# Kernel tuning notes

Hardware: AMD Instinct MI355X
Metric: run time of the kernel (lower is better)

The kernel has to match this reference:

```python
import jax, jax.numpy as jnp
import numpy as np

EPS = 1e-5

def conv(x, w, groups=1):
    # x: NCHW, w: OIHW, VALID padding, stride 1 (cross-correlation, same as torch conv2d)
    return jax.lax.conv_general_dilated(x, w, (1, 1), 'VALID',
                                        feature_group_count=groups,
                                        dimension_numbers=('NCHW', 'OIHW', 'NCHW'))

def bn(x, g, b, m, v):
    # eval-mode batchnorm with running stats
    scale = (g / jnp.sqrt(v + EPS))[None, :, None, None]
    return (x - m[None, :, None, None]) * scale + b[None, :, None, None]

def xcorr_depthwise(x, k):
    # x: [B,C,Hs,Ws] search, k: [B,C,Hk,Wk] per-sample kernels
    B, C, H, W = x.shape
    xr = x.reshape(1, B * C, H, W)
    kr = k.reshape(B * C, 1, k.shape[2], k.shape[3])
    out = conv(xr, kr, groups=B * C)  # [1, B*C, Ho, Wo]
    return out.reshape(B, C, out.shape[2], out.shape[3])

def setup_inputs() -> dict:
    key = jax.random.key(0)
    ks = jax.random.split(key, 16)
    Cin, Hid, Cout = 256, 256, 20
    inp = {
        'kernel': jax.random.normal(ks[0], (128, Cin, 7, 7), jnp.float32),
        'search': jax.random.normal(ks[1], (128, Cin, 31, 31), jnp.float32),
        'wk': jax.random.normal(ks[2], (Hid, Cin, 3, 3), jnp.float32) * 0.02,
        'gk': jnp.ones((Hid,), jnp.float32),
        'bk': jnp.zeros((Hid,), jnp.float32),
        'mk': jax.random.normal(ks[3], (Hid,), jnp.float32) * 0.1,
        'vk': jax.random.uniform(ks[4], (Hid,), jnp.float32) + 0.5,
        'ws': jax.random.normal(ks[5], (Hid, Cin, 3, 3), jnp.float32) * 0.02,
        'gs': jnp.ones((Hid,), jnp.float32),
        'bs': jnp.zeros((Hid,), jnp.float32),
        'ms': jax.random.normal(ks[6], (Hid,), jnp.float32) * 0.1,
        'vs': jax.random.uniform(ks[7], (Hid,), jnp.float32) + 0.5,
        'wh1': jax.random.normal(ks[8], (Hid, Hid, 1, 1), jnp.float32) * 0.02,
        'gh': jnp.ones((Hid,), jnp.float32),
        'bh': jnp.zeros((Hid,), jnp.float32),
        'mh': jax.random.normal(ks[9], (Hid,), jnp.float32) * 0.1,
        'vh': jax.random.uniform(ks[10], (Hid,), jnp.float32) + 0.5,
        'wh2': jax.random.normal(ks[11], (Cout, Hid, 1, 1), jnp.float32) * 0.02,
        'bh2': jnp.zeros((Cout,), jnp.float32),
    }
    return inp

def reference(kernel, search, wk, gk, bk, mk, vk, ws, gs, bs, ms, vs,
              wh1, gh, bh, mh, vh, wh2, bh2):
    k = jax.nn.relu(bn(conv(kernel, wk), gk, bk, mk, vk))   # [B,256,5,5]
    s = jax.nn.relu(bn(conv(search, ws), gs, bs, ms, vs))   # [B,256,29,29]
    f = xcorr_depthwise(s, k)                               # [B,256,25,25]
    h = jax.nn.relu(bn(conv(f, wh1), gh, bh, mh, vh))
    out = conv(h, wh2) + bh2[None, :, None, None]           # [B,20,25,25]
    return out
```

## Files before the change

### kernel.cpp

```cpp
#include <hip/hip_runtime.h>

typedef __bf16 bf16x8 __attribute__((ext_vector_type(8)));
typedef float floatx4 __attribute__((ext_vector_type(4)));
typedef unsigned short u16;
typedef unsigned int u32;

__device__ __forceinline__ u16 f2bf(float f) {
    union { float f; unsigned int u; } q; q.f = f;
    unsigned int r = q.u + 0x7FFFu + ((q.u >> 16) & 1u);
    return (u16)(r >> 16);
}
__device__ __forceinline__ float bf2f(u16 b) {
    union { unsigned int u; float f; } q; q.u = ((unsigned int)b) << 16;
    return q.f;
}

__device__ __forceinline__ void gl2lds16(const u16* g, u16* l) {
    __builtin_amdgcn_global_load_lds((const __attribute__((address_space(1))) u32*)g,
                                     (__attribute__((address_space(3))) u32*)l, 16, 0, 0);
}


__global__ __launch_bounds__(256) void bn_prep(
    const float* __restrict__ gk, const float* __restrict__ bk,
    const float* __restrict__ mk, const float* __restrict__ vk,
    const float* __restrict__ gs, const float* __restrict__ bs,
    const float* __restrict__ ms, const float* __restrict__ vs,
    const float* __restrict__ gh, const float* __restrict__ bh,
    const float* __restrict__ mh, const float* __restrict__ vh,
    float* __restrict__ par)
{
    int i = threadIdx.x;
    float s;
    s = gk[i] * rsqrtf(vk[i] + 1e-5f); par[0*256+i] = s; par[1*256+i] = bk[i] - mk[i]*s;
    s = gs[i] * rsqrtf(vs[i] + 1e-5f); par[2*256+i] = s; par[3*256+i] = bs[i] - ms[i]*s;
    s = gh[i] * rsqrtf(vh[i] + 1e-5f); par[4*256+i] = s; par[5*256+i] = bh[i] - mh[i]*s;
}

__global__ __launch_bounds__(256) void pack3x3(const float* __restrict__ w, u16* __restrict__ out) {
    int tid = blockIdx.x * 256 + threadIdx.x;
    int o  = tid / 2304;
    int k  = tid - o * 2304;
    int rc = k >> 8;
    int ci = k & 255;
    out[tid] = f2bf(w[o * 2304 + ci * 9 + rc]);
}

__global__ __launch_bounds__(256) void cast_bf16(const float* __restrict__ in, u16* __restrict__ out, int n) {
    int tid = blockIdx.x * 256 + threadIdx.x;
    if (tid < n) out[tid] = f2bf(in[tid]);
}

__global__ __launch_bounds__(256) void nchw2nhwc_t(const float* __restrict__ in, u16* __restrict__ out,
                                                   int HW, int sptiles) {
    __shared__ float tile[64][33];
    int bid = blockIdx.x;
    int st  = bid % sptiles;
    int tmp = bid / sptiles;
    int ct  = tmp & 3;
    int b   = tmp >> 2;
    int sp0 = st * 32, ci0 = ct * 64;
    int t = threadIdx.x;
    int j = t & 31, i8 = t >> 5;
    const float* ip = in + ((size_t)b * 256 + ci0 + i8) * HW + sp0 + j;
#pragma unroll
    for (int k = 0; k < 8; ++k) {
        if (sp0 + j < HW) tile[i8 + k * 8][j] = ip[(size_t)(k * 8) * HW];
    }
    __syncthreads();
    int cl = t & 63, s4 = t >> 6;
#pragma unroll
    for (int k = 0; k < 8; ++k) {
        int spl = s4 + k * 4;
        int sp  = sp0 + spl;
        if (sp < HW) out[((size_t)b * HW + sp) * 256 + ci0 + cl] = f2bf(tile[cl][spl]);
    }
}

__global__ __launch_bounds__(256) void conv_gemm(
    const u16* __restrict__ Ain, const u16* __restrict__ Wpk,
    const float* __restrict__ scale, const float* __restrict__ shift,
    u16* __restrict__ Out,
    int OHW, int OW, int IW, int bstride, int KW, int nrc, int mblocks)
{
    __shared__ u16 Alds[4096];
    __shared__ u16 Blds[4096];

    const int tot = mblocks * 2;
    const int grp = (tot >> 3) << 3;
    const int lid = blockIdx.x;
    const int nid = (lid < grp) ? ((lid & 7) * (grp >> 3) + (lid >> 3)) : lid;
    const int m0 = (nid >> 1) * 128;
    const int n0 = (nid & 1) * 128;

    const int t    = threadIdx.x;
    const int wave = t >> 6;
    const int lane = t & 63;
    const int quad = lane >> 4;
    const int lrow = lane & 15;

    const int koff = (((t & 3) ^ ((t >> 3) & 3)) << 3);
    const int r0 = t >> 2;
    int m_a0 = m0 + r0;
    int b0 = m_a0 / OHW; int rem0 = m_a0 - b0 * OHW; int y0 = rem0 / OW; int x0 = rem0 - y0 * OW;
    int m_a1 = m_a0 + 64;
    int b1 = m_a1 / OHW; int rem1 = m_a1 - b1 * OHW; int y1 = rem1 / OW; int x1 = rem1 - y1 * OW;
    const u16* ag0 = Ain + (size_t)b0 * bstride + (size_t)(y0 * IW + x0) * 256 + koff;
    const u16* ag1 = Ain + (size_t)b1 * bstride + (size_t)(y1 * IW + x1) * 256 + koff;
    const int Ktot = nrc * 256;
    const u16* bg0 = Wpk + (size_t)(n0 + r0) * Ktot + koff;
    const u16* bg1 = bg0 + (size_t)64 * Ktot;

    u16* lA0 = Alds + wave * 512;
    u16* lA1 = Alds + 2048 + wave * 512;
    u16* lB0 = Blds + wave * 512;
    u16* lB1 = Blds + 2048 + wave * 512;

    floatx4 zero = {0.f, 0.f, 0.f, 0.f};
    floatx4 acc[4][4];
#pragma unroll
    for (int i = 0; i < 4; ++i)
#pragma unroll
        for (int j = 0; j < 4; ++j) acc[i][j] = zero;

    const int wr  = (wave >> 1) << 6;
    const int wc  = (wave & 1) << 6;
    const int pos = ((quad ^ ((lrow >> 1) & 3)) << 3);

    const int nchunks = nrc << 3;
    for (int ch = 0; ch < nchunks; ++ch) {
        int rc  = ch >> 3;
        int ci0 = (ch & 7) << 5;
        int rr  = rc / KW;
        int cc  = rc - rr * KW;
        int ao  = (rr * IW + cc) * 256 + ci0;
        int bo  = ch << 5;
        __syncthreads();
        gl2lds16(ag0 + ao, lA0);
        gl2lds16(ag1 + ao, lA1);
        gl2lds16(bg0 + bo, lB0);
        gl2lds16(bg1 + bo, lB1);
        __syncthreads();
        bf16x8 af[4], bfr[4];
#pragma unroll
        for (int mi = 0; mi < 4; ++mi)
            af[mi] = *(const bf16x8*)&Alds[(wr + mi * 16 + lrow) * 32 + pos];
#pragma unroll
        for (int ni = 0; ni < 4; ++ni)
            bfr[ni] = *(const bf16x8*)&Blds[(wc + ni * 16 + lrow) * 32 + pos];
#pragma unroll
        for (int mi = 0; mi < 4; ++mi)
#pragma unroll
            for (int ni = 0; ni < 4; ++ni)
                acc[mi][ni] = __builtin_amdgcn_mfma_f32_16x16x32_bf16(af[mi], bfr[ni], acc[mi][ni], 0, 0, 0);
    }

    float sc[4], sh[4];
#pragma unroll
    for (int ni = 0; ni < 4; ++ni) {
        int gn = n0 + wc + ni * 16 + lrow;
        sc[ni] = scale[gn];
        sh[ni] = shift[gn];
    }
#pragma unroll
    for (int mi = 0; mi < 4; ++mi) {
        int gm = m0 + wr + mi * 16 + (quad << 2);
#pragma unroll
        for (int ri = 0; ri < 4; ++ri) {
            size_t ro = (size_t)(gm + ri) * 256 + n0 + wc + lrow;
#pragma unroll
            for (int ni = 0; ni < 4; ++ni) {
                float v = acc[mi][ni][ri] * sc[ni] + sh[ni];
                v = fmaxf(v, 0.f);
                Out[ro + ni * 16] = f2bf(v);
            }
        }
    }
}

__global__ __launch_bounds__(512, 2) void conv_gemm256(
    const u16* __restrict__ Ain, const u16* __restrict__ Wpk,
    const float* __restrict__ scale, const float* __restrict__ shift,
    u16* __restrict__ Out,
    int OHW, int OW, int IW, int bstride, int KW, int NKT, int Mtot)
{
    __shared__ __align__(16) u16 Alds[2][256][64];
    __shared__ __align__(16) u16 Blds[2][256][64];

    const int Ktot = NKT << 6;

    const int nblk = gridDim.x;
    const int lid = blockIdx.x;
    const int q8 = nblk >> 3, r8 = nblk & 7;
    const int xcd = lid & 7, sub = lid >> 3;
    const int nid = (xcd < r8) ? (xcd * (q8 + 1) + sub)
                               : (r8 * (q8 + 1) + (xcd - r8) * q8 + sub);
    const int m0 = nid << 8;

    const int t     = threadIdx.x;
    const int wave  = t >> 6;
    const int lane  = t & 63;
    const int lrow  = lane & 15;
    const int lquad = lane >> 4;
    const int wmBase = (wave >> 2) << 7;
    const int wnBase = (wave & 3) << 6;

    const u16* pA[4];
    const u16* pB[4];
#pragma unroll
    for (int j = 0; j < 4; ++j) {
        int u = j * 512 + t;
        int row = u >> 3, slot = u & 7;
        int ko = ((slot ^ (row & 7)) << 3);
        int m = m0 + row; if (m >= Mtot) m = Mtot - 1;
        int b = m / OHW; int rem = m - b * OHW; int y = rem / OW; int x = rem - y * OW;
        pA[j] = Ain + (size_t)b * bstride + (size_t)(y * IW + x) * 256 + ko;
        pB[j] = Wpk + (size_t)row * (size_t)Ktot + ko;
    }

    const int xo0 = ((lquad ^ (lrow & 7)) << 3);
    const int xo1 = xo0 ^ 32;

    floatx4 acc[8][4];
#pragma unroll
    for (int i = 0; i < 8; ++i)
#pragma unroll
        for (int j = 0; j < 4; ++j) acc[i][j] = (floatx4){0.f, 0.f, 0.f, 0.f};

#pragma unroll
    for (int j = 0; j < 4; ++j)
        gl2lds16(pA[j], &Alds[0][0][0] + j * 4096 + wave * 512);
#pragma unroll
    for (int j = 0; j < 4; ++j)
        gl2lds16(pB[j], &Blds[0][0][0] + j * 4096 + wave * 512);
    asm volatile("s_waitcnt vmcnt(0)" ::: "memory");
    __builtin_amdgcn_s_barrier();

#define LOADA(mb) do {                                              \
        const u16* _p = Ab + (wmBase + (mb) * 16 + lrow) * 64;      \
        aF[0][0] = *(const bf16x8*)(_p + xo0);                      \
        aF[0][1] = *(const bf16x8*)(_p + xo1);                      \
        aF[1][0] = *(const bf16x8*)(_p + 1024 + xo0);               \
        aF[1][1] = *(const bf16x8*)(_p + 1024 + xo1);               \
    } while (0)

#define MFMA16(mb) do {                                                                               \
        _Pragma("unroll")                                                                             \
        for (int _n = 0; _n < 4; ++_n) {                                                              \
            acc[(mb)][_n]     = __builtin_amdgcn_mfma_f32_16x16x32_bf16(aF[0][0], bB[_n][0], acc[(mb)][_n], 0, 0, 0);     \
            acc[(mb)][_n]     = __builtin_amdgcn_mfma_f32_16x16x32_bf16(aF[0][1], bB[_n][1], acc[(mb)][_n], 0, 0, 0);     \
            acc[(mb) + 1][_n] = __builtin_amdgcn_mfma_f32_16x16x32_bf16(aF[1][0], bB[_n][0], acc[(mb) + 1][_n], 0, 0, 0); \
            acc[(mb) + 1][_n] = __builtin_amdgcn_mfma_f32_16x16x32_bf16(aF[1][1], bB[_n][1], acc[(mb) + 1][_n], 0, 0, 0); \
        }                                                                                             \
    } while (0)

#define PH_MID() do {                                        \
        __builtin_amdgcn_s_barrier();                        \
        asm volatile("s_waitcnt lgkmcnt(0)" ::: "memory");   \
        __builtin_amdgcn_s_setprio(1);                       \
    } while (0)

#define PH_END() do {                                        \
        __builtin_amdgcn_s_setprio(0);                       \
        __builtin_amdgcn_s_barrier();                        \
    } while (0)

#pragma unroll 2
    for (int kt = 0; kt < NKT; ++kt) {
        const int c = kt & 1;
        const u16* Ab = &Alds[c][0][0];
        const u16* Bb = &Blds[c][0][0];
        u16* An = &Alds[c ^ 1][0][0];
        u16* Bn = &Blds[c ^ 1][0][0];
        const int pf = (kt + 1 < NKT);
        const int kt1 = kt + 1;
        const int rc = kt1 >> 2;
        const int rr = rc / KW;
        const int cc = rc - rr * KW;
        const int aoffA = (rr * IW + cc) * 256 + ((kt1 & 3) << 6);
        const int boffB = kt1 << 6;

        bf16x8 bB[4][2];
        bf16x8 aF[2][2];

#pragma unroll
        for (int ni = 0; ni < 4; ++ni) {
            const u16* _p = Bb + (wnBase + ni * 16 + lrow) * 64;
            bB[ni][0] = *(const bf16x8*)(_p + xo0);
            bB[ni][1] = *(const bf16x8*)(_p + xo1);
        }
        LOADA(0);
        if (pf) {
#pragma unroll
            for (int j = 0; j < 4; ++j)
                gl2lds16(pA[j] + aoffA, An + j * 4096 + wave * 512);
        }
        PH_MID();
        MFMA16(0);
        PH_END();

        LOADA(2);
        if (pf) {
#pragma unroll
            for (int j = 0; j < 4; ++j)
                gl2lds16(pB[j] + boffB, Bn + j * 4096 + wave * 512);
        }
        PH_MID();
        MFMA16(2);
        PH_END();

        LOADA(4);
        PH_MID();
        MFMA16(4);
        PH_END();

        LOADA(6);
        PH_MID();
        MFMA16(6);
        __builtin_amdgcn_s_setprio(0);
        asm volatile("s_waitcnt vmcnt(0)" ::: "memory");
        __builtin_amdgcn_s_barrier();
    }

#undef LOADA
#undef MFMA16
#undef PH_MID
#undef PH_END

    float sc[4], sh[4];
#pragma unroll
    for (int ni = 0; ni < 4; ++ni) {
        int gn = wnBase + ni * 16 + lrow;
        sc[ni] = scale[gn];
        sh[ni] = shift[gn];
    }
#pragma unroll
    for (int mi = 0; mi < 8; ++mi) {
        int gm0 = m0 + wmBase + mi * 16 + (lquad << 2);
#pragma unroll
        for (int ri = 0; ri < 4; ++ri) {
            int gm = gm0 + ri;
            if (gm < Mtot) {
                size_t ro = (size_t)gm * 256 + wnBase + lrow;
#pragma unroll
                for (int ni = 0; ni < 4; ++ni) {
                    float v = acc[mi][ni][ri] * sc[ni] + sh[ni];
                    v = fmaxf(v, 0.f);
                    Out[ro + ni * 16] = f2bf(v);
                }
            }
        }
    }
}

__global__ __launch_bounds__(256) void xcorr(const u16* __restrict__ ss, const u16* __restrict__ kk,
                                             u16* __restrict__ f) {
    int bid = blockIdx.x;
    int b = bid / 25, y = bid - b * 25;
    int ci = threadIdx.x;
    float kv[25];
#pragma unroll
    for (int i = 0; i < 25; ++i)
        kv[i] = bf2f(kk[(size_t)(b * 25 + i) * 256 + ci]);
    const u16* sbase = ss + (size_t)(b * 29 + y) * 29 * 256 + ci;
    u16* fbase = f + (size_t)(b * 25 + y) * 25 * 256 + ci;
    for (int x = 0; x < 25; ++x) {
        float acc = 0.f;
#pragma unroll
        for (int r = 0; r < 5; ++r)
#pragma unroll
            for (int c = 0; c < 5; ++c)
                acc += bf2f(sbase[(r * 29 + x + c) * 256]) * kv[r * 5 + c];
        fbase[x * 256] = f2bf(acc);
    }
}

__global__ __launch_bounds__(256) void head(const u16* __restrict__ h, const float* __restrict__ w2,
                                            const float* __restrict__ b2, float* __restrict__ out) {
    __shared__ u16   hl[25 * 264];
    __shared__ float wl[20 * 257];
    int bid = blockIdx.x;
    int b = bid / 25, y = bid - b * 25;
    int t = threadIdx.x;
    const u16* hrow = h + (size_t)(b * 25 + y) * 25 * 256;
    for (int i = t; i < 6400; i += 256) {
        int x = i >> 8, c = i & 255;
        hl[x * 264 + c] = hrow[i];
    }
    for (int i = t; i < 5120; i += 256) {
        int co = i >> 8, c = i & 255;
        wl[co * 257 + c] = w2[i];
    }
    __syncthreads();
    for (int o = t; o < 500; o += 256) {
        int x = o / 20, co = o - x * 20;
        float acc = b2[co];
        const u16* hp = &hl[x * 264];
        const float* wp = &wl[co * 257];
        for (int k = 0; k < 256; ++k) acc += bf2f(hp[k]) * wp[k];
        out[(size_t)((b * 20 + co) * 25 + y) * 25 + x] = acc;
    }
}

#define OFF_SIN  0ull
#define SZ_SIN   62980096ull
#define OFF_KIN  (OFF_SIN + SZ_SIN)
#define SZ_KIN   3211264ull
#define OFF_WKP  (OFF_KIN + SZ_KIN)
#define SZ_WKP   1179648ull
#define OFF_WSP  (OFF_WKP + SZ_WKP)
#define SZ_WSP   1179648ull
#define OFF_WH1P (OFF_WSP + SZ_WSP)
#define SZ_WH1P  131072ull
#define OFF_PAR  (OFF_WH1P + SZ_WH1P)
#define SZ_PAR   8192ull
#define OFF_KK   (OFF_PAR + SZ_PAR)
#define SZ_KK    1638400ull
#define OFF_SS   (OFF_KK + SZ_KK)
#define SZ_SS    55115776ull
#define OFF_F    OFF_SIN
#define OFF_H    OFF_SS

extern "C" void kernel_launch(void* const* d_in, const int* in_sizes, int n_in,
                              void* d_out, int out_size, void* d_ws, size_t ws_size,
                              hipStream_t stream) {
    const float* kin  = (const float*)d_in[0];
    const float* sin_ = (const float*)d_in[1];
    const float* wk   = (const float*)d_in[2];
    const float* gk   = (const float*)d_in[3];
    const float* bk   = (const float*)d_in[4];
    const float* mk   = (const float*)d_in[5];
    const float* vk   = (const float*)d_in[6];
    const float* wsw  = (const float*)d_in[7];
    const float* gs   = (const float*)d_in[8];
    const float* bs   = (const float*)d_in[9];
    const float* ms   = (const float*)d_in[10];
    const float* vs   = (const float*)d_in[11];
    const float* wh1  = (const float*)d_in[12];
    const float* gh   = (const float*)d_in[13];
    const float* bh   = (const float*)d_in[14];
    const float* mh   = (const float*)d_in[15];
    const float* vh   = (const float*)d_in[16];
    const float* wh2  = (const float*)d_in[17];
    const float* bh2  = (const float*)d_in[18];
    float* out = (float*)d_out;

    char* w = (char*)d_ws;
    u16*   SIN  = (u16*)(w + OFF_SIN);
    u16*   KIN  = (u16*)(w + OFF_KIN);
    u16*   WKP  = (u16*)(w + OFF_WKP);
    u16*   WSP  = (u16*)(w + OFF_WSP);
    u16*   WH1P = (u16*)(w + OFF_WH1P);
    float* PAR  = (float*)(w + OFF_PAR);
    u16*   KK   = (u16*)(w + OFF_KK);
    u16*   SS   = (u16*)(w + OFF_SS);
    u16*   F    = (u16*)(w + OFF_F);
    u16*   H    = (u16*)(w + OFF_H);

    bn_prep<<<1, 256, 0, stream>>>(gk, bk, mk, vk, gs, bs, ms, vs, gh, bh, mh, vh, PAR);
    pack3x3<<<2304, 256, 0, stream>>>(wk, WKP);
    pack3x3<<<2304, 256, 0, stream>>>(wsw, WSP);
    cast_bf16<<<256, 256, 0, stream>>>(wh1, WH1P, 65536);
    nchw2nhwc_t<<<128 * 4 * 2, 256, 0, stream>>>(kin, KIN, 49, 2);
    nchw2nhwc_t<<<128 * 4 * 31, 256, 0, stream>>>(sin_, SIN, 961, 31);

    conv_gemm<<<50, 256, 0, stream>>>(KIN, WKP, PAR + 0, PAR + 256, KK,
                                      25, 5, 7, 12544, 3, 9, 25);
    conv_gemm256<<<421, 512, 0, stream>>>(SIN, WSP, PAR + 512, PAR + 768, SS,
                                          841, 29, 31, 246016, 3, 36, 107648);
    xcorr<<<3200, 256, 0, stream>>>(SS, KK, F);
    conv_gemm<<<1250, 256, 0, stream>>>(F, WH1P, PAR + 1024, PAR + 1280, H,
                                        625, 25, 25, 160000, 1, 1, 625);
    head<<<3200, 256, 0, stream>>>(H, wh2, bh2, out);

    (void)in_sizes; (void)n_in; (void)out_size; (void)ws_size;
}
```

Baseline: 573.3 us.

## Split A-tile prefetch across phases and vectorize depthwise xcorr loads

In the conv GEMM main loop, the prefetch of the next B tile is issued first and the A tile prefetch is split into two halves issued in different phases. A mid-loop barrier now uses a partial vmcnt wait, so a barrier only waits for the loads the next phase needs, which is meant to spread global-to-LDS traffic and shorten stalls. Separately, the xcorr kernel is rewritten so each thread handles 8 channels with 16-byte bf16x8 loads and stores across 4 output columns, replacing scalar 2-byte accesses. The vmcnt counts have to match exactly which loads are in flight. Any mismatch could race on LDS or break correctness.

```diff
diff --git a/kernel.cpp b/kernel.cpp
--- a/kernel.cpp
+++ b/kernel.cpp
@@ -229,10 +229,11 @@
 
 #pragma unroll
     for (int j = 0; j < 4; ++j)
-        gl2lds16(pA[j], &Alds[0][0][0] + j * 4096 + wave * 512);
-#pragma unroll
-    for (int j = 0; j < 4; ++j)
         gl2lds16(pB[j], &Blds[0][0][0] + j * 4096 + wave * 512);
+    gl2lds16(pA[0], &Alds[0][0][0] + 0 * 4096 + wave * 512);
+    gl2lds16(pA[2], &Alds[0][0][0] + 2 * 4096 + wave * 512);
+    gl2lds16(pA[1], &Alds[0][0][0] + 1 * 4096 + wave * 512);
+    gl2lds16(pA[3], &Alds[0][0][0] + 3 * 4096 + wave * 512);
     asm volatile("s_waitcnt vmcnt(0)" ::: "memory");
     __builtin_amdgcn_s_barrier();
 
@@ -293,7 +294,7 @@
         if (pf) {
 #pragma unroll
             for (int j = 0; j < 4; ++j)
-                gl2lds16(pA[j] + aoffA, An + j * 4096 + wave * 512);
+                gl2lds16(pB[j] + boffB, Bn + j * 4096 + wave * 512);
         }
         PH_MID();
         MFMA16(0);
@@ -301,15 +302,21 @@
 
         LOADA(2);
         if (pf) {
-#pragma unroll
-            for (int j = 0; j < 4; ++j)
-                gl2lds16(pB[j] + boffB, Bn + j * 4096 + wave * 512);
+            gl2lds16(pA[0] + aoffA, An + 0 * 4096 + wave * 512);
+            gl2lds16(pA[2] + aoffA, An + 2 * 4096 + wave * 512);
         }
         PH_MID();
         MFMA16(2);
-        PH_END();
+        __builtin_amdgcn_s_setprio(0);
+        if (pf) asm volatile("s_waitcnt vmcnt(6)" ::: "memory");
+        else    asm volatile("s_waitcnt vmcnt(0)" ::: "memory");
+        __builtin_amdgcn_s_barrier();
 
         LOADA(4);
+        if (pf) {
+            gl2lds16(pA[1] + aoffA, An + 1 * 4096 + wave * 512);
+            gl2lds16(pA[3] + aoffA, An + 3 * 4096 + wave * 512);
+        }
         PH_MID();
         MFMA16(4);
         PH_END();
@@ -318,7 +325,8 @@
         PH_MID();
         MFMA16(6);
         __builtin_amdgcn_s_setprio(0);
-        asm volatile("s_waitcnt vmcnt(0)" ::: "memory");
+        if (pf) asm volatile("s_waitcnt vmcnt(2)" ::: "memory");
+        else    asm volatile("s_waitcnt vmcnt(0)" ::: "memory");
         __builtin_amdgcn_s_barrier();
     }
 
@@ -357,21 +365,49 @@
                                              u16* __restrict__ f) {
     int bid = blockIdx.x;
     int b = bid / 25, y = bid - b * 25;
-    int ci = threadIdx.x;
-    float kv[25];
-#pragma unroll
-    for (int i = 0; i < 25; ++i)
-        kv[i] = bf2f(kk[(size_t)(b * 25 + i) * 256 + ci]);
-    const u16* sbase = ss + (size_t)(b * 29 + y) * 29 * 256 + ci;
-    u16* fbase = f + (size_t)(b * 25 + y) * 25 * 256 + ci;
-    for (int x = 0; x < 25; ++x) {
-        float acc = 0.f;
-#pragma unroll
-        for (int r = 0; r < 5; ++r)
-#pragma unroll
-            for (int c = 0; c < 5; ++c)
-                acc += bf2f(sbase[(r * 29 + x + c) * 256]) * kv[r * 5 + c];
-        fbase[x * 256] = f2bf(acc);
+    int t = threadIdx.x;
+    int cg = (t & 31) << 3;
+    int xg = t >> 5;
+    const u16* kbase = kk + (size_t)b * 25 * 256 + cg;
+    const u16* sbase = ss + (size_t)(b * 29 + y) * 29 * 256 + cg;
+
+    float acc[4][8];
+#pragma unroll
+    for (int j = 0; j < 4; ++j)
+#pragma unroll
+        for (int e = 0; e < 8; ++e) acc[j][e] = 0.f;
+
+#pragma unroll
+    for (int r = 0; r < 5; ++r) {
+        const u16* srow = sbase + (size_t)r * 29 * 256;
+#pragma unroll
+        for (int c = 0; c < 5; ++c) {
+            bf16x8 kv = *(const bf16x8*)(kbase + (r * 5 + c) * 256);
+            float kf[8];
+#pragma unroll
+            for (int e = 0; e < 8; ++e) kf[e] = (float)kv[e];
+#pragma unroll
+            for (int j = 0; j < 4; ++j) {
+                int x = xg + 8 * j;
+                if (x < 25) {
+                    bf16x8 sv = *(const bf16x8*)(srow + (size_t)(x + c) * 256);
+#pragma unroll
+                    for (int e = 0; e < 8; ++e) acc[j][e] += (float)sv[e] * kf[e];
+                }
+            }
+        }
+    }
+
+    u16* fb = f + (size_t)(b * 25 + y) * 25 * 256 + cg;
+#pragma unroll
+    for (int j = 0; j < 4; ++j) {
+        int x = xg + 8 * j;
+        if (x < 25) {
+            u16 pk[8];
+#pragma unroll
+            for (int e = 0; e < 8; ++e) pk[e] = f2bf(acc[j][e]);
+            *(bf16x8*)(fb + (size_t)x * 256) = *(const bf16x8*)pk;
+        }
     }
 }
 
```

After: 595.5 us. 3.9% more time.
